# Performance work log

Measured on AMD Instinct MI355X. Metric: run time of the kernel, lower is better.

The kernel has to match this reference:

```python
import jax, jax.numpy as jnp
import numpy as np

LN_EPS = 1e-5

def _layernorm(x, g, b):
    mu = jnp.mean(x, axis=-1, keepdims=True)
    var = jnp.var(x, axis=-1, keepdims=True)
    return (x - mu) * jax.lax.rsqrt(var + LN_EPS) * g + b

def setup_inputs() -> dict:
    key = jax.random.key(0)
    ks = jax.random.split(key, 8)
    B, N, C, OUT, H = 2, 512, 256, 256, 4
    s_in = 1.0 / np.sqrt(C)
    s_2c = 1.0 / np.sqrt(2 * C)
    s_out = 1.0 / np.sqrt(OUT)
    return {
        "x": jax.random.normal(ks[0], (B, N, C), jnp.float32),
        "We": jax.random.uniform(ks[1], (2 * C, OUT), jnp.float32, -s_2c, s_2c),
        "be": jnp.zeros((OUT,), jnp.float32),
        "ln1_g": jnp.ones((OUT,), jnp.float32),
        "ln1_b": jnp.zeros((OUT,), jnp.float32),
        "W2": jax.random.uniform(ks[2], (OUT, H), jnp.float32, -s_out, s_out),
        "b2": jnp.zeros((H,), jnp.float32),
        "Wv": jax.random.uniform(ks[3], (C, OUT), jnp.float32, -s_in, s_in),
        "bv": jnp.zeros((OUT,), jnp.float32),
        "Wo": jax.random.uniform(ks[4], (OUT, OUT), jnp.float32, -s_out, s_out),
        "bo": jnp.zeros((OUT,), jnp.float32),
        "ln2_g": jnp.ones((OUT,), jnp.float32),
        "ln2_b": jnp.zeros((OUT,), jnp.float32),
    }

def reference(x, We, be, ln1_g, ln1_b, W2, b2, Wv, bv, Wo, bo, ln2_g, ln2_b):
    B, N, C = x.shape
    OUT = We.shape[1]
    H = W2.shape[1]
    hd = OUT // H
    # edge MLP first Linear on concat([x_i, x_j]) == x_i@We[:C] + x_j@We[C:] + be
    h_i = x @ We[:C] + be          # [B,N,OUT]
    h_j = x @ We[C:]               # [B,N,OUT]
    e = h_i[:, :, None, :] + h_j[:, None, :, :]   # [B,Ni,Nj,OUT]
    e = jax.nn.gelu(_layernorm(e, ln1_g, ln1_b), approximate=False)
    logits = e @ W2 + b2                           # [B,Ni,Nj,H]
    adj = jax.nn.softmax(logits, axis=2)           # softmax over Nj
    v = (x @ Wv + bv).reshape(B, N, H, hd)         # [B,N,H,hd]
    out = jnp.einsum('bijh,bjhd->bihd', adj, v).reshape(B, N, OUT)
    out = out @ Wo + bo
    return _layernorm(out + x, ln2_g, ln2_b)
```

## Files before the change

### kernel.cpp

```cpp
#include <hip/hip_runtime.h>
#include <math.h>

#define NB    2
#define NN    512
#define CC    256
#define OUTC  256
#define HH    4
#define LN_EPS 1e-5f

#define WS_HI     0
#define WS_HJ     262144
#define WS_V      524288
#define WS_LOGITS 786432
#define WS_CROSS  2883584
#define WS_SI     3407872
#define WS_SSI    3408896
#define WS_SJ     3409920
#define WS_SSJ    3410944

__device__ __forceinline__ float gelu_fast(float x) {
    float s = x * x;
    float w = fmaf(-0.1029432f, s, -2.3022077f);
    float e = exp2f(x * w);
    return x * __builtin_amdgcn_rcpf(1.0f + e);
}

__global__ __launch_bounds__(256) void kA(
    const float* __restrict__ x,  const float* __restrict__ We,
    const float* __restrict__ be, const float* __restrict__ Wv,
    const float* __restrict__ bv,
    float* __restrict__ hi, float* __restrict__ hj, float* __restrict__ v,
    float* __restrict__ Si, float* __restrict__ SSi,
    float* __restrict__ Sj, float* __restrict__ SSj)
{
    __shared__ __align__(16) float xs[4][CC];
    const int r0 = blockIdx.x * 4;
    const int t  = threadIdx.x;
    #pragma unroll
    for (int k = 0; k < 4; ++k)
        xs[k][t] = x[(size_t)(r0 + k) * CC + t];
    __syncthreads();

    const int w = t >> 6, l = t & 63;
    const int r = r0 + w;
    const float* __restrict__ xrow = xs[w];
    const float4* __restrict__ We0 = (const float4*)We + l;
    const float4* __restrict__ We1 = (const float4*)(We + (size_t)CC * OUTC) + l;
    const float4* __restrict__ Wv4 = (const float4*)Wv + l;

    float4 ai = {0,0,0,0}, aj = {0,0,0,0}, av = {0,0,0,0};
    #pragma unroll 4
    for (int c = 0; c < CC; ++c) {
        float xv = xrow[c];
        float4 a = We0[(size_t)c * 64];
        float4 bq = We1[(size_t)c * 64];
        float4 cq = Wv4[(size_t)c * 64];
        ai.x = fmaf(xv, a.x, ai.x); ai.y = fmaf(xv, a.y, ai.y);
        ai.z = fmaf(xv, a.z, ai.z); ai.w = fmaf(xv, a.w, ai.w);
        aj.x = fmaf(xv, bq.x, aj.x); aj.y = fmaf(xv, bq.y, aj.y);
        aj.z = fmaf(xv, bq.z, aj.z); aj.w = fmaf(xv, bq.w, aj.w);
        av.x = fmaf(xv, cq.x, av.x); av.y = fmaf(xv, cq.y, av.y);
        av.z = fmaf(xv, cq.z, av.z); av.w = fmaf(xv, cq.w, av.w);
    }
    float4 be4 = ((const float4*)be)[l];
    float4 bv4 = ((const float4*)bv)[l];
    float4 hiv = make_float4(ai.x + be4.x, ai.y + be4.y, ai.z + be4.z, ai.w + be4.w);
    float4 vv  = make_float4(av.x + bv4.x, av.y + bv4.y, av.z + bv4.z, av.w + bv4.w);

    ((float4*)hi)[(size_t)r * 64 + l] = hiv;
    ((float4*)hj)[(size_t)r * 64 + l] = aj;
    ((float4*)v )[(size_t)r * 64 + l] = vv;

    float si = (hiv.x + hiv.y) + (hiv.z + hiv.w);
    float ssi = hiv.x * hiv.x;
    ssi = fmaf(hiv.y, hiv.y, ssi); ssi = fmaf(hiv.z, hiv.z, ssi); ssi = fmaf(hiv.w, hiv.w, ssi);
    float sj = (aj.x + aj.y) + (aj.z + aj.w);
    float ssj = aj.x * aj.x;
    ssj = fmaf(aj.y, aj.y, ssj); ssj = fmaf(aj.z, aj.z, ssj); ssj = fmaf(aj.w, aj.w, ssj);
    #pragma unroll
    for (int off = 1; off < 64; off <<= 1) {
        si  += __shfl_xor(si,  off);
        ssi += __shfl_xor(ssi, off);
        sj  += __shfl_xor(sj,  off);
        ssj += __shfl_xor(ssj, off);
    }
    if (l == 0) { Si[r] = si; SSi[r] = ssi; Sj[r] = sj; SSj[r] = ssj; }
}

#define LXP 260
__global__ __launch_bounds__(256) void kX(
    const float* __restrict__ hi, const float* __restrict__ hj,
    float* __restrict__ cross)
{
    __shared__ __align__(16) float his[32][LXP];
    __shared__ __align__(16) float hjs[32][LXP];
    const int bid = blockIdx.x;
    const int b  = bid >> 8;
    const int i0 = ((bid >> 4) & 15) * 32;
    const int j0 = (bid & 15) * 32;
    const int t  = threadIdx.x;

    const float4* srcA = (const float4*)(hi + ((size_t)b * NN + i0) * OUTC);
    const float4* srcB = (const float4*)(hj + ((size_t)b * NN + j0) * OUTC);
    #pragma unroll
    for (int k = 0; k < 8; ++k) {
        int s = k * 256 + t, row = s >> 6, c4 = s & 63;
        *(float4*)&his[row][c4 * 4] = srcA[s];
        *(float4*)&hjs[row][c4 * 4] = srcB[s];
    }
    __syncthreads();

    const int oi = (t & 15) * 2, oj = (t >> 4) * 2;
    float a00 = 0.f, a01 = 0.f, a10 = 0.f, a11 = 0.f;
    #pragma unroll 2
    for (int c4 = 0; c4 < 64; ++c4) {
        float4 A0 = *(const float4*)&his[oi    ][c4 * 4];
        float4 A1 = *(const float4*)&his[oi + 1][c4 * 4];
        float4 B0 = *(const float4*)&hjs[oj    ][c4 * 4];
        float4 B1 = *(const float4*)&hjs[oj + 1][c4 * 4];
        a00 = fmaf(A0.x, B0.x, a00); a00 = fmaf(A0.y, B0.y, a00);
        a00 = fmaf(A0.z, B0.z, a00); a00 = fmaf(A0.w, B0.w, a00);
        a01 = fmaf(A0.x, B1.x, a01); a01 = fmaf(A0.y, B1.y, a01);
        a01 = fmaf(A0.z, B1.z, a01); a01 = fmaf(A0.w, B1.w, a01);
        a10 = fmaf(A1.x, B0.x, a10); a10 = fmaf(A1.y, B0.y, a10);
        a10 = fmaf(A1.z, B0.z, a10); a10 = fmaf(A1.w, B0.w, a10);
        a11 = fmaf(A1.x, B1.x, a11); a11 = fmaf(A1.y, B1.y, a11);
        a11 = fmaf(A1.z, B1.z, a11); a11 = fmaf(A1.w, B1.w, a11);
    }
    size_t base = ((size_t)b * NN + i0 + oi) * NN + j0 + oj;
    cross[base]          = a00;
    cross[base + 1]      = a01;
    cross[base + NN]     = a10;
    cross[base + NN + 1] = a11;
}

#define LDP 260
__global__ __launch_bounds__(256) void kB(
    const float* __restrict__ hi,  const float* __restrict__ hj,
    const float* __restrict__ ln1g, const float* __restrict__ ln1b,
    const float* __restrict__ W2,  const float* __restrict__ b2,
    const float* __restrict__ Si,  const float* __restrict__ SSi,
    const float* __restrict__ Sj,  const float* __restrict__ SSj,
    const float* __restrict__ cross,
    float* __restrict__ logits)
{
    __shared__ __align__(16) float hjs[32][LDP];
    __shared__ __align__(16) float his[8][LDP];
    __shared__ __align__(16) float g1s[CC];
    __shared__ __align__(16) float b1s[CC];
    __shared__ __align__(16) float w2s[CC][HH];
    __shared__ __align__(16) float crs[256];
    __shared__ float sis[8], ssis[8], sjs[32], ssjs[32];

    const int bid = blockIdx.x;
    const int jt  = (bid & 15) * 32;
    const int it  = ((bid >> 4) & 63) * 8;
    const int b   = bid >> 10;
    const int t   = threadIdx.x;

    {
        const float4* src = (const float4*)(hj + (size_t)(b * NN + jt) * OUTC);
        #pragma unroll
        for (int k = 0; k < 8; ++k) {
            int s = k * 256 + t, row = s >> 6, c4 = s & 63;
            *(float4*)&hjs[row][c4 * 4] = src[s];
        }
    }
    {
        const float4* src = (const float4*)(hi + (size_t)(b * NN + it) * OUTC);
        #pragma unroll
        for (int k = 0; k < 2; ++k) {
            int s = k * 256 + t, row = s >> 6, c4 = s & 63;
            *(float4*)&his[row][c4 * 4] = src[s];
        }
    }
    g1s[t] = ln1g[t];
    b1s[t] = ln1b[t];
    #pragma unroll
    for (int k = 0; k < 4; ++k)
        ((float*)w2s)[t + 256 * k] = W2[t + 256 * k];
    crs[t] = cross[((size_t)(b * NN + it + (t >> 5))) * NN + jt + (t & 31)];
    if (t < 8)               { sis[t] = Si[b * NN + it + t];  ssis[t] = SSi[b * NN + it + t]; }
    if (t >= 64 && t < 96)   { int q = t - 64; sjs[q] = Sj[b * NN + jt + q]; ssjs[q] = SSj[b * NN + jt + q]; }
    __syncthreads();

    const int w = t >> 6, l = t & 63;
    const int il = 2 * w + (l >> 5);
    const int jl = l & 31;
    const int i = it + il;
    const int j = jt + jl;
    const float* __restrict__ hirow = &his[il][0];
    const float* __restrict__ hjrow = &hjs[jl][0];

    const float mu  = (sis[il] + sjs[jl]) * (1.f / 256.f);
    const float msq = fmaf(2.f, crs[(il << 5) + jl], ssis[il] + ssjs[jl]) * (1.f / 256.f);
    const float var = fmaf(-mu, mu, msq);
    const float rs  = rsqrtf(var + LN_EPS);
    const float nmurs = -mu * rs;

    float p0 = 0.f, p1 = 0.f, p2 = 0.f, p3 = 0.f;
    #pragma unroll 4
    for (int c4 = 0; c4 < 64; ++c4) {
        float4 a  = *(const float4*)&hirow[c4 * 4];
        float4 bb = *(const float4*)&hjrow[c4 * 4];
        float4 g  = ((const float4*)g1s)[c4];
        float4 be_ = ((const float4*)b1s)[c4];
        const float4* w2r = (const float4*)&w2s[c4 * 4][0];
        {
            float n = fmaf(a.x + bb.x, rs, nmurs);
            n = fmaf(n, g.x, be_.x);
            float ge = gelu_fast(n);
            float4 wr = w2r[0];
            p0 = fmaf(ge, wr.x, p0); p1 = fmaf(ge, wr.y, p1);
            p2 = fmaf(ge, wr.z, p2); p3 = fmaf(ge, wr.w, p3);
        }
        {
            float n = fmaf(a.y + bb.y, rs, nmurs);
            n = fmaf(n, g.y, be_.y);
            float ge = gelu_fast(n);
            float4 wr = w2r[1];
            p0 = fmaf(ge, wr.x, p0); p1 = fmaf(ge, wr.y, p1);
            p2 = fmaf(ge, wr.z, p2); p3 = fmaf(ge, wr.w, p3);
        }
        {
            float n = fmaf(a.z + bb.z, rs, nmurs);
            n = fmaf(n, g.z, be_.z);
            float ge = gelu_fast(n);
            float4 wr = w2r[2];
            p0 = fmaf(ge, wr.x, p0); p1 = fmaf(ge, wr.y, p1);
            p2 = fmaf(ge, wr.z, p2); p3 = fmaf(ge, wr.w, p3);
        }
        {
            float n = fmaf(a.w + bb.w, rs, nmurs);
            n = fmaf(n, g.w, be_.w);
            float ge = gelu_fast(n);
            float4 wr = w2r[3];
            p0 = fmaf(ge, wr.x, p0); p1 = fmaf(ge, wr.y, p1);
            p2 = fmaf(ge, wr.z, p2); p3 = fmaf(ge, wr.w, p3);
        }
    }
    float4 b2v = *(const float4*)b2;
    float4 outv = make_float4(p0 + b2v.x, p1 + b2v.y, p2 + b2v.z, p3 + b2v.w);
    ((float4*)logits)[(size_t)(b * NN + i) * NN + j] = outv;
}

__global__ __launch_bounds__(256) void kC(
    const float* __restrict__ logits, const float* __restrict__ v,
    const float* __restrict__ Wo,     const float* __restrict__ bo,
    const float* __restrict__ x,      const float* __restrict__ g2,
    const float* __restrict__ b2ln,   float* __restrict__ out)
{
    __shared__ __align__(16) float wl[2][NN * HH];
    __shared__ __align__(16) float sm[2][HH][2];
    __shared__ __align__(16) float out1[2][OUTC];
    __shared__ float redb[4][2][2];

    const int bid = blockIdx.x;
    const int b   = bid >> 8;
    const int i0  = (bid & 255) * 2;
    const int t   = threadIdx.x;

    {
        const float4* src = (const float4*)(logits + ((size_t)b * NN + i0) * NN * HH);
        float4* dst = (float4*)wl;
        #pragma unroll
        for (int k = 0; k < 4; ++k) dst[k * 256 + t] = src[k * 256 + t];
    }
    __syncthreads();

    {
        const int g = t >> 5, k = t & 31;
        const int row = g >> 2, h = g & 3;
        const float* base = wl[row] + h;
        float m = -1e30f;
        #pragma unroll
        for (int mm = 0; mm < 16; ++mm) m = fmaxf(m, base[(k + 32 * mm) * 4]);
        #pragma unroll
        for (int off = 1; off < 32; off <<= 1) m = fmaxf(m, __shfl_xor(m, off, 32));
        float ssum = 0.f;
        #pragma unroll
        for (int mm = 0; mm < 16; ++mm) ssum += __expf(base[(k + 32 * mm) * 4] - m);
        #pragma unroll
        for (int off = 1; off < 32; off <<= 1) ssum += __shfl_xor(ssum, off, 32);
        if (k == 0) { sm[row][h][0] = m; sm[row][h][1] = 1.f / ssum; }
    }
    __syncthreads();

    {
        float* wlf = &wl[0][0];
        #pragma unroll 4
        for (int k = 0; k < 16; ++k) {
            int idx = t + 256 * k;
            int row = idx >> 11, h = idx & 3;
            wlf[idx] = __expf(wlf[idx] - sm[row][h][0]) * sm[row][h][1];
        }
    }
    __syncthreads();

    {
        const int h = t >> 6;
        float a0 = 0.f, a1 = 0.f;
        const float* vb = v + (size_t)b * NN * OUTC + t;
        const float* p0 = wl[0] + h;
        const float* p1 = wl[1] + h;
        #pragma unroll 8
        for (int j = 0; j < NN; ++j) {
            float vv = vb[(size_t)j * OUTC];
            a0 = fmaf(p0[j * 4], vv, a0);
            a1 = fmaf(p1[j * 4], vv, a1);
        }
        out1[0][t] = a0; out1[1][t] = a1;
    }
    __syncthreads();

    {
        float a0 = bo[t], a1 = a0;
        #pragma unroll 4
        for (int c = 0; c < OUTC; ++c) {
            float wv = Wo[(size_t)c * OUTC + t];
            a0 = fmaf(out1[0][c], wv, a0);
            a1 = fmaf(out1[1][c], wv, a1);
        }
        float r0v = a0 + x[((size_t)b * NN + i0    ) * OUTC + t];
        float r1v = a1 + x[((size_t)b * NN + i0 + 1) * OUTC + t];

        const int w = t >> 6, l = t & 63;
        float sv0 = r0v, sq0 = r0v * r0v, sv1 = r1v, sq1 = r1v * r1v;
        #pragma unroll
        for (int off = 1; off < 64; off <<= 1) {
            sv0 += __shfl_xor(sv0, off); sq0 += __shfl_xor(sq0, off);
            sv1 += __shfl_xor(sv1, off); sq1 += __shfl_xor(sq1, off);
        }
        if (l == 0) {
            redb[w][0][0] = sv0; redb[w][0][1] = sq0;
            redb[w][1][0] = sv1; redb[w][1][1] = sq1;
        }
        __syncthreads();
        float gg = g2[t], bb = b2ln[t];
        {
            float sv = redb[0][0][0] + redb[1][0][0] + redb[2][0][0] + redb[3][0][0];
            float sq = redb[0][0][1] + redb[1][0][1] + redb[2][0][1] + redb[3][0][1];
            float mu = sv * (1.f / 256.f);
            float var = sq * (1.f / 256.f) - mu * mu;
            float rsi = rsqrtf(var + LN_EPS);
            out[((size_t)b * NN + i0) * OUTC + t] = (r0v - mu) * rsi * gg + bb;
        }
        {
            float sv = redb[0][1][0] + redb[1][1][0] + redb[2][1][0] + redb[3][1][0];
            float sq = redb[0][1][1] + redb[1][1][1] + redb[2][1][1] + redb[3][1][1];
            float mu = sv * (1.f / 256.f);
            float var = sq * (1.f / 256.f) - mu * mu;
            float rsi = rsqrtf(var + LN_EPS);
            out[((size_t)b * NN + i0 + 1) * OUTC + t] = (r1v - mu) * rsi * gg + bb;
        }
    }
}

extern "C" void kernel_launch(void* const* d_in, const int* in_sizes, int n_in,
                              void* d_out, int out_size, void* d_ws, size_t ws_size,
                              hipStream_t stream) {
    (void)in_sizes; (void)n_in; (void)out_size; (void)ws_size;
    const float* x    = (const float*)d_in[0];
    const float* We   = (const float*)d_in[1];
    const float* be   = (const float*)d_in[2];
    const float* ln1g = (const float*)d_in[3];
    const float* ln1b = (const float*)d_in[4];
    const float* W2   = (const float*)d_in[5];
    const float* b2   = (const float*)d_in[6];
    const float* Wv   = (const float*)d_in[7];
    const float* bv   = (const float*)d_in[8];
    const float* Wo   = (const float*)d_in[9];
    const float* bo   = (const float*)d_in[10];
    const float* ln2g = (const float*)d_in[11];
    const float* ln2b = (const float*)d_in[12];
    float* out = (float*)d_out;

    float* ws = (float*)d_ws;
    float* hi     = ws + WS_HI;
    float* hj     = ws + WS_HJ;
    float* v      = ws + WS_V;
    float* logits = ws + WS_LOGITS;
    float* cross  = ws + WS_CROSS;
    float* Si     = ws + WS_SI;
    float* SSi    = ws + WS_SSI;
    float* Sj     = ws + WS_SJ;
    float* SSj    = ws + WS_SSJ;

    kA<<<256,  256, 0, stream>>>(x, We, be, Wv, bv, hi, hj, v, Si, SSi, Sj, SSj);
    kX<<<512,  256, 0, stream>>>(hi, hj, cross);
    kB<<<2048, 256, 0, stream>>>(hi, hj, ln1g, ln1b, W2, b2,
                                 Si, SSi, Sj, SSj, cross, logits);
    kC<<<512,  256, 0, stream>>>(logits, v, Wo, bo, x, ln2g, ln2b, out);
}
```

Measured before the change: 241.6 us.

## Restructure projection kernel to reuse weight loads across eight rows per block

The projection kernel now processes 8 rows per block. Each thread owns one output column and accumulates all 8 rows, so every weight element loaded is reused 8 times instead of once per row, and the grid shrinks from 256 to 128 blocks. Row sum and sum-of-squares statistics are reduced with wave shuffles followed by a small shared-memory cross-wave step. Separately, the GELU exponential switches to the raw hardware exp2 builtin. The costs are fewer blocks on a large GPU, more registers for the 8-row accumulators, and 32 shuffle reductions per wave.

Result: faster. 219.3 us (-9.2%).

```diff
diff --git a/kernel.cpp b/kernel.cpp
--- a/kernel.cpp
+++ b/kernel.cpp
@@ -21,7 +21,7 @@
 __device__ __forceinline__ float gelu_fast(float x) {
     float s = x * x;
     float w = fmaf(-0.1029432f, s, -2.3022077f);
-    float e = exp2f(x * w);
+    float e = __builtin_amdgcn_exp2f(x * w);
     return x * __builtin_amdgcn_rcpf(1.0f + e);
 }
 
@@ -33,58 +33,70 @@
     float* __restrict__ Si, float* __restrict__ SSi,
     float* __restrict__ Sj, float* __restrict__ SSj)
 {
-    __shared__ __align__(16) float xs[4][CC];
-    const int r0 = blockIdx.x * 4;
+    __shared__ __align__(16) float xs[8][CC];
+    __shared__ float red[4][32];
+    const int r0 = blockIdx.x * 8;
     const int t  = threadIdx.x;
-    #pragma unroll
-    for (int k = 0; k < 4; ++k)
-        xs[k][t] = x[(size_t)(r0 + k) * CC + t];
-    __syncthreads();
-
-    const int w = t >> 6, l = t & 63;
-    const int r = r0 + w;
-    const float* __restrict__ xrow = xs[w];
-    const float4* __restrict__ We0 = (const float4*)We + l;
-    const float4* __restrict__ We1 = (const float4*)(We + (size_t)CC * OUTC) + l;
-    const float4* __restrict__ Wv4 = (const float4*)Wv + l;
-
-    float4 ai = {0,0,0,0}, aj = {0,0,0,0}, av = {0,0,0,0};
+
+    {
+        const float4* src = (const float4*)(x + (size_t)r0 * CC);
+        #pragma unroll
+        for (int k = 0; k < 2; ++k)
+            ((float4*)xs)[k * 256 + t] = src[k * 256 + t];
+    }
+    __syncthreads();
+
+    float hia[8] = {0,0,0,0,0,0,0,0};
+    float hja[8] = {0,0,0,0,0,0,0,0};
+    float va [8] = {0,0,0,0,0,0,0,0};
     #pragma unroll 4
     for (int c = 0; c < CC; ++c) {
-        float xv = xrow[c];
-        float4 a = We0[(size_t)c * 64];
-        float4 bq = We1[(size_t)c * 64];
-        float4 cq = Wv4[(size_t)c * 64];
-        ai.x = fmaf(xv, a.x, ai.x); ai.y = fmaf(xv, a.y, ai.y);
-        ai.z = fmaf(xv, a.z, ai.z); ai.w = fmaf(xv, a.w, ai.w);
-        aj.x = fmaf(xv, bq.x, aj.x); aj.y = fmaf(xv, bq.y, aj.y);
-        aj.z = fmaf(xv, bq.z, aj.z); aj.w = fmaf(xv, bq.w, aj.w);
-        av.x = fmaf(xv, cq.x, av.x); av.y = fmaf(xv, cq.y, av.y);
-        av.z = fmaf(xv, cq.z, av.z); av.w = fmaf(xv, cq.w, av.w);
-    }
-    float4 be4 = ((const float4*)be)[l];
-    float4 bv4 = ((const float4*)bv)[l];
-    float4 hiv = make_float4(ai.x + be4.x, ai.y + be4.y, ai.z + be4.z, ai.w + be4.w);
-    float4 vv  = make_float4(av.x + bv4.x, av.y + bv4.y, av.z + bv4.z, av.w + bv4.w);
-
-    ((float4*)hi)[(size_t)r * 64 + l] = hiv;
-    ((float4*)hj)[(size_t)r * 64 + l] = aj;
-    ((float4*)v )[(size_t)r * 64 + l] = vv;
-
-    float si = (hiv.x + hiv.y) + (hiv.z + hiv.w);
-    float ssi = hiv.x * hiv.x;
-    ssi = fmaf(hiv.y, hiv.y, ssi); ssi = fmaf(hiv.z, hiv.z, ssi); ssi = fmaf(hiv.w, hiv.w, ssi);
-    float sj = (aj.x + aj.y) + (aj.z + aj.w);
-    float ssj = aj.x * aj.x;
-    ssj = fmaf(aj.y, aj.y, ssj); ssj = fmaf(aj.z, aj.z, ssj); ssj = fmaf(aj.w, aj.w, ssj);
+        float we0 = We[(size_t)c * OUTC + t];
+        float we1 = We[(size_t)(CC + c) * OUTC + t];
+        float wv  = Wv[(size_t)c * OUTC + t];
+        #pragma unroll
+        for (int r = 0; r < 8; ++r) {
+            float xv = xs[r][c];
+            hia[r] = fmaf(xv, we0, hia[r]);
+            hja[r] = fmaf(xv, we1, hja[r]);
+            va [r] = fmaf(xv, wv , va [r]);
+        }
+    }
+    float beT = be[t], bvT = bv[t];
     #pragma unroll
-    for (int off = 1; off < 64; off <<= 1) {
-        si  += __shfl_xor(si,  off);
-        ssi += __shfl_xor(ssi, off);
-        sj  += __shfl_xor(sj,  off);
-        ssj += __shfl_xor(ssj, off);
-    }
-    if (l == 0) { Si[r] = si; SSi[r] = ssi; Sj[r] = sj; SSj[r] = ssj; }
+    for (int r = 0; r < 8; ++r) {
+        hia[r] += beT;
+        va [r] += bvT;
+        hi[(size_t)(r0 + r) * OUTC + t] = hia[r];
+        hj[(size_t)(r0 + r) * OUTC + t] = hja[r];
+        v [(size_t)(r0 + r) * OUTC + t] = va [r];
+    }
+
+    const int w = t >> 6, l = t & 63;
+    float part[32];
+    #pragma unroll
+    for (int r = 0; r < 8; ++r) {
+        part[r * 4 + 0] = hia[r];
+        part[r * 4 + 1] = hia[r] * hia[r];
+        part[r * 4 + 2] = hja[r];
+        part[r * 4 + 3] = hja[r] * hja[r];
+    }
+    #pragma unroll
+    for (int q = 0; q < 32; ++q) {
+        float s = part[q];
+        #pragma unroll
+        for (int off = 1; off < 64; off <<= 1) s += __shfl_xor(s, off);
+        if (l == 0) red[w][q] = s;
+    }
+    __syncthreads();
+    if (t < 32) {
+        float s = red[0][t] + red[1][t] + red[2][t] + red[3][t];
+        int r = r0 + (t >> 2), st = t & 3;
+        if      (st == 0) Si [r] = s;
+        else if (st == 1) SSi[r] = s;
+        else if (st == 2) Sj [r] = s;
+        else              SSj[r] = s;
+    }
 }
 
 #define LXP 260
@@ -386,7 +398,7 @@
     float* Sj     = ws + WS_SJ;
     float* SSj    = ws + WS_SSJ;
 
-    kA<<<256,  256, 0, stream>>>(x, We, be, Wv, bv, hi, hj, v, Si, SSi, Sj, SSj);
+    kA<<<128,  256, 0, stream>>>(x, We, be, Wv, bv, hi, hj, v, Si, SSi, Sj, SSj);
     kX<<<512,  256, 0, stream>>>(hi, hj, cross);
     kB<<<2048, 256, 0, stream>>>(hi, hj, ln1g, ln1b, W2, b2,
                                  Si, SSi, Sj, SSj, cross, logits);
```
